# Performance work log

Hardware: AMD Instinct MI355X
Metric: run time of the kernel (lower is better)

## Reference

```python
import jax, jax.numpy as jnp
import numpy as np

BN_EPS = 1e-5


def setup_inputs() -> dict:
    key = jax.random.key(0)
    ks = jax.random.split(key, 8)
    b, c, h, w, d = 16, 256, 128, 128, 64
    x = jax.random.normal(ks[0], (b, c, h, w), dtype=jnp.float32)
    conv1_w = jax.random.normal(ks[1], (c, c), dtype=jnp.float32) * np.sqrt(2.0 / c)
    conv1_b = jax.random.normal(ks[2], (c,), dtype=jnp.float32) * 0.02
    mk_w = jax.random.normal(ks[3], (d, c), dtype=jnp.float32) * np.sqrt(2.0 / d)
    mv_w = jnp.transpose(mk_w)  # original ties mv.weight = mk.weight.permute(1,0,2)
    conv2_w = jax.random.normal(ks[4], (c, c), dtype=jnp.float32) * np.sqrt(2.0 / c)
    bn_gamma = jnp.ones((c,), dtype=jnp.float32)
    bn_beta = jnp.zeros((c,), dtype=jnp.float32)
    bn_mean = jax.random.normal(ks[5], (c,), dtype=jnp.float32) * 0.1
    bn_var = jax.random.uniform(ks[6], (c,), dtype=jnp.float32, minval=0.5, maxval=1.5)
    return {"x": x, "conv1_w": conv1_w, "conv1_b": conv1_b, "mk_w": mk_w,
            "mv_w": mv_w, "conv2_w": conv2_w, "bn_gamma": bn_gamma,
            "bn_beta": bn_beta, "bn_mean": bn_mean, "bn_var": bn_var}


def reference(x, conv1_w, conv1_b, mk_w, mv_w, conv2_w, bn_gamma, bn_beta, bn_mean, bn_var):
    b, c, h, w = x.shape
    n = h * w
    identity = x
    # conv1: 1x1 conv with bias -> [b, c, n]
    y = jnp.einsum('oc,bchw->bohw', conv1_w, x) + conv1_b[None, :, None, None]
    y = y.reshape(b, c, n)
    # external attention: mk projection [b, d, n]
    attn = jnp.einsum('dc,bcn->bdn', mk_w, y)
    attn = jax.nn.softmax(attn, axis=-1)              # softmax over spatial N
    attn = attn / (1e-9 + attn.sum(axis=1, keepdims=True))  # column-normalize over d
    # mv projection back to channels [b, c, n]
    z = jnp.einsum('cd,bdn->bcn', mv_w, attn)
    z = z.reshape(b, c, h, w)
    # conv2 (1x1, no bias) + BatchNorm (inference) + residual + relu
    z = jnp.einsum('oc,bchw->bohw', conv2_w, z)
    inv = bn_gamma / jnp.sqrt(bn_var + BN_EPS)
    z = z * inv[None, :, None, None] + (bn_beta - bn_mean * inv)[None, :, None, None]
    return jax.nn.relu(z + identity)
```

## Files before the change

### kernel.cpp

```cpp
#include <hip/hip_runtime.h>

#define HW 16384
#define C  256
#define D  64
#define NB 16

typedef unsigned short u16;
typedef __attribute__((ext_vector_type(4))) float  f32x4;
typedef __attribute__((ext_vector_type(4))) short  s16x4;
typedef __attribute__((ext_vector_type(8))) short  s16x8;

__device__ __forceinline__ float fast_exp(float v) {
    return exp2f(v * 1.44269504088896340736f);
}
__device__ __forceinline__ float bf2f(u16 u) {
    return __uint_as_float(((unsigned int)u) << 16);
}
__device__ __forceinline__ u16 f2bf(float f) {
    unsigned int u = __float_as_uint(f);
    unsigned int r = (u + 0x7fffu + ((u >> 16) & 1u)) >> 16;
    return (u16)r;
}

#define MFMA16(a, b, c) __builtin_amdgcn_mfma_f32_16x16x32_bf16((a), (b), (c), 0, 0, 0)

__global__ void precompute_kernel(const float* __restrict__ conv1_w,
                                  const float* __restrict__ conv1_b,
                                  const float* __restrict__ mk_w,
                                  const float* __restrict__ mv_w,
                                  const float* __restrict__ conv2_w,
                                  const float* __restrict__ gamma,
                                  const float* __restrict__ beta,
                                  const float* __restrict__ mean,
                                  const float* __restrict__ var,
                                  short* __restrict__ Ath,
                                  short* __restrict__ Atl,
                                  float* __restrict__ amk,
                                  short* __restrict__ Bmb,
                                  float* __restrict__ shift)
{
    int gid = blockIdx.x * blockDim.x + threadIdx.x;
    if (gid < C * D) {
        int d = gid >> 8, cp = gid & 255;
        float s = 0.f;
        for (int c = 0; c < C; ++c) s += mk_w[d * C + c] * conv1_w[c * C + cp];
        u16 h = f2bf(s);
        Ath[gid] = (short)h;
        Atl[gid] = (short)f2bf(s - bf2f(h));
    } else if (gid < 2 * C * D) {
        int g = gid - C * D;
        int o = g >> 6, d = g & 63;
        float inv = gamma[o] * rsqrtf(var[o] + 1e-5f);
        float s = 0.f;
        for (int c = 0; c < C; ++c) s += conv2_w[o * C + c] * mv_w[c * D + d];
        Bmb[g] = (short)f2bf(s * inv);
    } else if (gid < 2 * C * D + D) {
        int d = gid - 2 * C * D;
        float s = 0.f;
        for (int c = 0; c < C; ++c) s += mk_w[d * C + c] * conv1_b[c];
        amk[d] = s;
    } else if (gid < 2 * C * D + D + C) {
        int o = gid - (2 * C * D + D);
        float inv = gamma[o] * rsqrtf(var[o] + 1e-5f);
        shift[o] = beta[o] - mean[o] * inv;
    }
}

#define NT1 64
__global__ __launch_bounds__(256, 2) void logits_kernel(const float* __restrict__ x,
                                                        const short* __restrict__ Ath,
                                                        const short* __restrict__ Atl,
                                                        const float* __restrict__ amk,
                                                        u16* __restrict__ logits)
{
    __shared__ short xs[NT1][2 * C + 8];
    const int t = threadIdx.x;
    const int b = blockIdx.y;
    const int n0 = blockIdx.x * NT1;
    const int lane = t & 63, w = t >> 6;
    const int col = lane & 15, g = lane >> 4;

    s16x8 Ah[8], Al[8];
    {
        const short* ah = Ath + (size_t)(w * 16 + col) * C + 8 * g;
        const short* al = Atl + (size_t)(w * 16 + col) * C + 8 * g;
        #pragma unroll
        for (int ks = 0; ks < 8; ++ks) {
            Ah[ks] = *(const s16x8*)(ah + ks * 32);
            Al[ks] = *(const s16x8*)(al + ks * 32);
        }
    }

    const float* xb = x + (size_t)b * C * HW + n0;
    #pragma unroll
    for (int i = 0; i < 4; ++i) {
        int cell = i * 256 + t;
        int nq = cell & 15, cq = cell >> 4;
        int c0 = cq * 4, nn = nq * 4;
        const float* gp = xb + (size_t)c0 * HW + nn;
        f32x4 r0 = *(const f32x4*)(gp);
        f32x4 r1 = *(const f32x4*)(gp + HW);
        f32x4 r2 = *(const f32x4*)(gp + 2 * HW);
        f32x4 r3 = *(const f32x4*)(gp + 3 * HW);
        #pragma unroll
        for (int j = 0; j < 4; ++j) {
            float v0 = r0[j], v1 = r1[j], v2 = r2[j], v3 = r3[j];
            u16 h0 = f2bf(v0), h1 = f2bf(v1), h2 = f2bf(v2), h3 = f2bf(v3);
            s16x4 hi = { (short)h0, (short)h1, (short)h2, (short)h3 };
            s16x4 lo = { (short)f2bf(v0 - bf2f(h0)), (short)f2bf(v1 - bf2f(h1)),
                         (short)f2bf(v2 - bf2f(h2)), (short)f2bf(v3 - bf2f(h3)) };
            *(s16x4*)&xs[nn + j][c0]     = hi;
            *(s16x4*)&xs[nn + j][C + c0] = lo;
        }
    }
    __syncthreads();

    f32x4 zz = {0.f, 0.f, 0.f, 0.f};
    f32x4 acc[4] = { zz, zz, zz, zz };
    #pragma unroll
    for (int ks = 0; ks < 8; ++ks) {
        #pragma unroll
        for (int nt = 0; nt < 4; ++nt) {
            const short* xr = &xs[nt * 16 + col][ks * 32 + 8 * g];
            s16x8 bh = *(const s16x8*)(xr);
            s16x8 bl = *(const s16x8*)(xr + C);
            acc[nt] = MFMA16(Ah[ks], bh, acc[nt]);
            acc[nt] = MFMA16(Al[ks], bh, acc[nt]);
            acc[nt] = MFMA16(Ah[ks], bl, acc[nt]);
        }
    }

    f32x4 av = *(const f32x4*)(amk + w * 16 + 4 * g);
    u16* lb = logits + (size_t)b * D * HW + n0;
    #pragma unroll
    for (int nt = 0; nt < 4; ++nt) {
        #pragma unroll
        for (int r = 0; r < 4; ++r) {
            int d = w * 16 + 4 * g + r;
            lb[(size_t)d * HW + nt * 16 + col] = f2bf(acc[nt][r] + av[r]);
        }
    }
}

__global__ __launch_bounds__(256) void stats_kernel(const u16* __restrict__ logits,
                                                    float* __restrict__ stats)
{
    const int row = blockIdx.x;
    const u16* lr = logits + (size_t)row * HW;
    const int t = threadIdx.x;
    const int lane = t & 63, wid = t >> 6;

    float v[64];
    float m = -3.402823466e+38f;
    #pragma unroll
    for (int i = 0; i < 64; ++i) {
        v[i] = bf2f(lr[t + i * 256]);
        m = fmaxf(m, v[i]);
    }
    #pragma unroll
    for (int off = 1; off < 64; off <<= 1) m = fmaxf(m, __shfl_xor(m, off));

    __shared__ float redm[4];
    if (lane == 0) redm[wid] = m;
    __syncthreads();
    const float bm = fmaxf(fmaxf(redm[0], redm[1]), fmaxf(redm[2], redm[3]));

    float s = 0.f;
    #pragma unroll
    for (int i = 0; i < 64; ++i) s += fast_exp(v[i] - bm);
    #pragma unroll
    for (int off = 1; off < 64; off <<= 1) s += __shfl_xor(s, off);

    __shared__ float reds[4];
    if (lane == 0) reds[wid] = s;
    __syncthreads();
    if (t == 0) {
        float S = reds[0] + reds[1] + reds[2] + reds[3];
        stats[2 * row]     = bm;
        stats[2 * row + 1] = 1.0f / S;
    }
}

#define NT3 128
__global__ __launch_bounds__(512, 4) void out_kernel(const float* __restrict__ x,
                                                     const u16* __restrict__ logits,
                                                     const float* __restrict__ stats,
                                                     const short* __restrict__ Bmb,
                                                     const float* __restrict__ shift,
                                                     float* __restrict__ out)
{
    __shared__ short ps[NT3][72];
    __shared__ float csum[4][NT3];
    __shared__ float rr[NT3];

    const int t = threadIdx.x;
    const int b = blockIdx.y;
    const int n0 = blockIdx.x * NT3;

    {
        const int nl = t & 127, dq = t >> 7;
        const u16* lg = logits + (size_t)b * D * HW + (size_t)(dq * 16) * HW + n0 + nl;
        const float* st = stats + 2 * (b * D + dq * 16);
        float cs = 0.f;
        #pragma unroll
        for (int j4 = 0; j4 < 4; ++j4) {
            s16x4 pk;
            #pragma unroll
            for (int jj = 0; jj < 4; ++jj) {
                int j = j4 * 4 + jj;
                float M = st[2 * j], invS = st[2 * j + 1];
                float pv = fast_exp(bf2f(lg[(size_t)j * HW]) - M) * invS;
                cs += pv;
                pk[jj] = (short)f2bf(pv);
            }
            *(s16x4*)&ps[nl][dq * 16 + j4 * 4] = pk;
        }
        csum[dq][nl] = cs;
    }
    __syncthreads();
    if (t < NT3) {
        float s = csum[0][t] + csum[1][t] + csum[2][t] + csum[3][t] + 1e-9f;
        rr[t] = 1.0f / s;
    }
    __syncthreads();

    const int lane = t & 63, col = lane & 15, g = lane >> 4;
    const int W = t >> 6, Wo = W >> 1, Wn = W & 1;

    s16x8 A[4][2];
    #pragma unroll
    for (int ot = 0; ot < 4; ++ot) {
        const short* bp = Bmb + (size_t)(Wo * 64 + ot * 16 + col) * D + 8 * g;
        A[ot][0] = *(const s16x8*)(bp);
        A[ot][1] = *(const s16x8*)(bp + 32);
    }

    f32x4 zz = {0.f, 0.f, 0.f, 0.f};
    f32x4 acc[4][4];
    #pragma unroll
    for (int ot = 0; ot < 4; ++ot)
        #pragma unroll
        for (int nt = 0; nt < 4; ++nt) acc[ot][nt] = zz;

    #pragma unroll
    for (int nt = 0; nt < 4; ++nt) {
        const short* pr = &ps[Wn * 64 + nt * 16 + col][8 * g];
        s16x8 b0 = *(const s16x8*)(pr);
        s16x8 b1 = *(const s16x8*)(pr + 32);
        #pragma unroll
        for (int ot = 0; ot < 4; ++ot) {
            acc[ot][nt] = MFMA16(A[ot][0], b0, acc[ot][nt]);
            acc[ot][nt] = MFMA16(A[ot][1], b1, acc[ot][nt]);
        }
    }

    const float* xb = x + (size_t)b * C * HW + n0;
    float* ob = out + (size_t)b * C * HW + n0;
    #pragma unroll
    for (int ot = 0; ot < 4; ++ot) {
        f32x4 sh = *(const f32x4*)(shift + Wo * 64 + ot * 16 + 4 * g);
        #pragma unroll
        for (int nt = 0; nt < 4; ++nt) {
            int nc = Wn * 64 + nt * 16 + col;
            float rv = rr[nc];
            #pragma unroll
            for (int r = 0; r < 4; ++r) {
                int o = Wo * 64 + ot * 16 + 4 * g + r;
                float xv = xb[(size_t)o * HW + nc];
                float v = acc[ot][nt][r] * rv + sh[r] + xv;
                ob[(size_t)o * HW + nc] = fmaxf(v, 0.f);
            }
        }
    }
}

extern "C" void kernel_launch(void* const* d_in, const int* in_sizes, int n_in,
                              void* d_out, int out_size, void* d_ws, size_t ws_size,
                              hipStream_t stream)
{
    const float* x       = (const float*)d_in[0];
    const float* conv1_w = (const float*)d_in[1];
    const float* conv1_b = (const float*)d_in[2];
    const float* mk_w    = (const float*)d_in[3];
    const float* mv_w    = (const float*)d_in[4];
    const float* conv2_w = (const float*)d_in[5];
    const float* gamma   = (const float*)d_in[6];
    const float* beta    = (const float*)d_in[7];
    const float* mean    = (const float*)d_in[8];
    const float* var     = (const float*)d_in[9];
    float* out = (float*)d_out;

    float* amk   = (float*)d_ws;
    float* shift = amk + D;
    float* stats = shift + C;
    short* Ath   = (short*)(stats + 2 * NB * D);
    short* Atl   = Ath + C * D;
    short* Bmb   = Atl + C * D;
    u16* logits  = (u16*)(Bmb + C * D);

    const int pre_work = 2 * C * D + D + C;
    precompute_kernel<<<(pre_work + 255) / 256, 256, 0, stream>>>(
        conv1_w, conv1_b, mk_w, mv_w, conv2_w, gamma, beta, mean, var,
        Ath, Atl, amk, Bmb, shift);

    logits_kernel<<<dim3(HW / NT1, NB), 256, 0, stream>>>(x, Ath, Atl, amk, logits);

    stats_kernel<<<NB * D, 256, 0, stream>>>(logits, stats);

    out_kernel<<<dim3(HW / NT3, NB), 512, 0, stream>>>(x, logits, stats, Bmb, shift, out);
}
```

Before: 581.8 us.

## Swap MFMA operand roles for vectorized stores, drop x low-part split

The logits kernel now converts x to a single bf16 plane instead of hi/lo planes. It swaps the MFMA operands so that each lane's accumulator holds contiguous spatial positions, which lets it write logits as 4-wide vector stores, and it loads the weights after the shared-memory fill to lower register pressure. The stats kernel reads logits four at a time, and the out kernel uses 64-column tiles with 256 threads and the swapped operand order, so residual loads and output stores become float4. The costs removed are scalar strided global accesses and one third of the logits MFMAs; in exchange x is kept only to bf16 precision (no low part), which loosens logit accuracy.

Result: no change. 588.1 us (+1.1%).

```diff
diff --git a/kernel.cpp b/kernel.cpp
--- a/kernel.cpp
+++ b/kernel.cpp
@@ -67,29 +67,19 @@
 }
 
 #define NT1 64
-__global__ __launch_bounds__(256, 2) void logits_kernel(const float* __restrict__ x,
+#define XR  (C + 8)
+__global__ __launch_bounds__(256, 3) void logits_kernel(const float* __restrict__ x,
                                                         const short* __restrict__ Ath,
                                                         const short* __restrict__ Atl,
                                                         const float* __restrict__ amk,
                                                         u16* __restrict__ logits)
 {
-    __shared__ short xs[NT1][2 * C + 8];
+    __shared__ short xs[NT1 * XR];
     const int t = threadIdx.x;
     const int b = blockIdx.y;
     const int n0 = blockIdx.x * NT1;
     const int lane = t & 63, w = t >> 6;
     const int col = lane & 15, g = lane >> 4;
-
-    s16x8 Ah[8], Al[8];
-    {
-        const short* ah = Ath + (size_t)(w * 16 + col) * C + 8 * g;
-        const short* al = Atl + (size_t)(w * 16 + col) * C + 8 * g;
-        #pragma unroll
-        for (int ks = 0; ks < 8; ++ks) {
-            Ah[ks] = *(const s16x8*)(ah + ks * 32);
-            Al[ks] = *(const s16x8*)(al + ks * 32);
-        }
-    }
 
     const float* xb = x + (size_t)b * C * HW + n0;
     #pragma unroll
@@ -104,16 +94,23 @@
         f32x4 r3 = *(const f32x4*)(gp + 3 * HW);
         #pragma unroll
         for (int j = 0; j < 4; ++j) {
-            float v0 = r0[j], v1 = r1[j], v2 = r2[j], v3 = r3[j];
-            u16 h0 = f2bf(v0), h1 = f2bf(v1), h2 = f2bf(v2), h3 = f2bf(v3);
-            s16x4 hi = { (short)h0, (short)h1, (short)h2, (short)h3 };
-            s16x4 lo = { (short)f2bf(v0 - bf2f(h0)), (short)f2bf(v1 - bf2f(h1)),
-                         (short)f2bf(v2 - bf2f(h2)), (short)f2bf(v3 - bf2f(h3)) };
-            *(s16x4*)&xs[nn + j][c0]     = hi;
-            *(s16x4*)&xs[nn + j][C + c0] = lo;
-        }
-    }
-    __syncthreads();
+            s16x4 hi = { (short)f2bf(r0[j]), (short)f2bf(r1[j]),
+                         (short)f2bf(r2[j]), (short)f2bf(r3[j]) };
+            *(s16x4*)&xs[(nn + j) * XR + c0] = hi;
+        }
+    }
+    __syncthreads();
+
+    s16x8 Ah[8], Al[8];
+    {
+        const short* ah = Ath + (size_t)(w * 16 + col) * C + 8 * g;
+        const short* al = Atl + (size_t)(w * 16 + col) * C + 8 * g;
+        #pragma unroll
+        for (int ks = 0; ks < 8; ++ks) {
+            Ah[ks] = *(const s16x8*)(ah + ks * 32);
+            Al[ks] = *(const s16x8*)(al + ks * 32);
+        }
+    }
 
     f32x4 zz = {0.f, 0.f, 0.f, 0.f};
     f32x4 acc[4] = { zz, zz, zz, zz };
@@ -121,24 +118,20 @@
     for (int ks = 0; ks < 8; ++ks) {
         #pragma unroll
         for (int nt = 0; nt < 4; ++nt) {
-            const short* xr = &xs[nt * 16 + col][ks * 32 + 8 * g];
-            s16x8 bh = *(const s16x8*)(xr);
-            s16x8 bl = *(const s16x8*)(xr + C);
-            acc[nt] = MFMA16(Ah[ks], bh, acc[nt]);
-            acc[nt] = MFMA16(Al[ks], bh, acc[nt]);
-            acc[nt] = MFMA16(Ah[ks], bl, acc[nt]);
-        }
-    }
-
-    f32x4 av = *(const f32x4*)(amk + w * 16 + 4 * g);
-    u16* lb = logits + (size_t)b * D * HW + n0;
+            s16x8 xf = *(const s16x8*)&xs[(nt * 16 + col) * XR + ks * 32 + 8 * g];
+            acc[nt] = MFMA16(xf, Ah[ks], acc[nt]);
+            acc[nt] = MFMA16(xf, Al[ks], acc[nt]);
+        }
+    }
+
+    const float am = amk[w * 16 + col];
+    u16* lb = logits + (size_t)b * D * HW + (size_t)(w * 16 + col) * HW + n0;
     #pragma unroll
     for (int nt = 0; nt < 4; ++nt) {
-        #pragma unroll
-        for (int r = 0; r < 4; ++r) {
-            int d = w * 16 + 4 * g + r;
-            lb[(size_t)d * HW + nt * 16 + col] = f2bf(acc[nt][r] + av[r]);
-        }
+        s16x4 st4;
+        #pragma unroll
+        for (int r = 0; r < 4; ++r) st4[r] = (short)f2bf(acc[nt][r] + am);
+        *(s16x4*)(lb + nt * 16 + 4 * g) = st4;
     }
 }
 
@@ -146,16 +139,21 @@
                                                     float* __restrict__ stats)
 {
     const int row = blockIdx.x;
-    const u16* lr = logits + (size_t)row * HW;
+    const s16x4* lr = (const s16x4*)(logits + (size_t)row * HW);
     const int t = threadIdx.x;
     const int lane = t & 63, wid = t >> 6;
 
     float v[64];
     float m = -3.402823466e+38f;
     #pragma unroll
-    for (int i = 0; i < 64; ++i) {
-        v[i] = bf2f(lr[t + i * 256]);
-        m = fmaxf(m, v[i]);
+    for (int i = 0; i < 16; ++i) {
+        s16x4 q = lr[t + i * 256];
+        #pragma unroll
+        for (int k = 0; k < 4; ++k) {
+            float f = bf2f((u16)q[k]);
+            v[i * 4 + k] = f;
+            m = fmaxf(m, f);
+        }
     }
     #pragma unroll
     for (int off = 1; off < 64; off <<= 1) m = fmaxf(m, __shfl_xor(m, off));
@@ -181,15 +179,15 @@
     }
 }
 
-#define NT3 128
-__global__ __launch_bounds__(512, 4) void out_kernel(const float* __restrict__ x,
+#define NT3 64
+__global__ __launch_bounds__(256, 3) void out_kernel(const float* __restrict__ x,
                                                      const u16* __restrict__ logits,
                                                      const float* __restrict__ stats,
                                                      const short* __restrict__ Bmb,
                                                      const float* __restrict__ shift,
                                                      float* __restrict__ out)
 {
-    __shared__ short ps[NT3][72];
+    __shared__ short ps[NT3 * 72];
     __shared__ float csum[4][NT3];
     __shared__ float rr[NT3];
 
@@ -198,7 +196,7 @@
     const int n0 = blockIdx.x * NT3;
 
     {
-        const int nl = t & 127, dq = t >> 7;
+        const int nl = t & 63, dq = t >> 6;
         const u16* lg = logits + (size_t)b * D * HW + (size_t)(dq * 16) * HW + n0 + nl;
         const float* st = stats + 2 * (b * D + dq * 16);
         float cs = 0.f;
@@ -208,31 +206,28 @@
             #pragma unroll
             for (int jj = 0; jj < 4; ++jj) {
                 int j = j4 * 4 + jj;
-                float M = st[2 * j], invS = st[2 * j + 1];
-                float pv = fast_exp(bf2f(lg[(size_t)j * HW]) - M) * invS;
+                float pv = fast_exp(bf2f(lg[(size_t)j * HW]) - st[2 * j]) * st[2 * j + 1];
                 cs += pv;
                 pk[jj] = (short)f2bf(pv);
             }
-            *(s16x4*)&ps[nl][dq * 16 + j4 * 4] = pk;
+            *(s16x4*)&ps[nl * 72 + dq * 16 + j4 * 4] = pk;
         }
         csum[dq][nl] = cs;
     }
     __syncthreads();
-    if (t < NT3) {
-        float s = csum[0][t] + csum[1][t] + csum[2][t] + csum[3][t] + 1e-9f;
-        rr[t] = 1.0f / s;
-    }
+    if (t < NT3)
+        rr[t] = 1.0f / (csum[0][t] + csum[1][t] + csum[2][t] + csum[3][t] + 1e-9f);
     __syncthreads();
 
     const int lane = t & 63, col = lane & 15, g = lane >> 4;
-    const int W = t >> 6, Wo = W >> 1, Wn = W & 1;
-
-    s16x8 A[4][2];
+    const int w = t >> 6;
+
+    s16x8 Bf[4][2];
     #pragma unroll
     for (int ot = 0; ot < 4; ++ot) {
-        const short* bp = Bmb + (size_t)(Wo * 64 + ot * 16 + col) * D + 8 * g;
-        A[ot][0] = *(const s16x8*)(bp);
-        A[ot][1] = *(const s16x8*)(bp + 32);
+        const short* bp = Bmb + (size_t)(w * 64 + ot * 16 + col) * D + 8 * g;
+        Bf[ot][0] = *(const s16x8*)(bp);
+        Bf[ot][1] = *(const s16x8*)(bp + 32);
     }
 
     f32x4 zz = {0.f, 0.f, 0.f, 0.f};
@@ -244,32 +239,34 @@
 
     #pragma unroll
     for (int nt = 0; nt < 4; ++nt) {
-        const short* pr = &ps[Wn * 64 + nt * 16 + col][8 * g];
-        s16x8 b0 = *(const s16x8*)(pr);
-        s16x8 b1 = *(const s16x8*)(pr + 32);
+        const short* pr = &ps[(nt * 16 + col) * 72 + 8 * g];
+        s16x8 p0 = *(const s16x8*)(pr);
+        s16x8 p1 = *(const s16x8*)(pr + 32);
         #pragma unroll
         for (int ot = 0; ot < 4; ++ot) {
-            acc[ot][nt] = MFMA16(A[ot][0], b0, acc[ot][nt]);
-            acc[ot][nt] = MFMA16(A[ot][1], b1, acc[ot][nt]);
-        }
-    }
+            acc[ot][nt] = MFMA16(p0, Bf[ot][0], acc[ot][nt]);
+            acc[ot][nt] = MFMA16(p1, Bf[ot][1], acc[ot][nt]);
+        }
+    }
+
+    float sh[4];
+    #pragma unroll
+    for (int ot = 0; ot < 4; ++ot) sh[ot] = shift[w * 64 + ot * 16 + col];
 
     const float* xb = x + (size_t)b * C * HW + n0;
     float* ob = out + (size_t)b * C * HW + n0;
     #pragma unroll
-    for (int ot = 0; ot < 4; ++ot) {
-        f32x4 sh = *(const f32x4*)(shift + Wo * 64 + ot * 16 + 4 * g);
-        #pragma unroll
-        for (int nt = 0; nt < 4; ++nt) {
-            int nc = Wn * 64 + nt * 16 + col;
-            float rv = rr[nc];
+    for (int nt = 0; nt < 4; ++nt) {
+        f32x4 rv = *(const f32x4*)&rr[nt * 16 + 4 * g];
+        #pragma unroll
+        for (int ot = 0; ot < 4; ++ot) {
+            const size_t off = (size_t)(w * 64 + ot * 16 + col) * HW + nt * 16 + 4 * g;
+            f32x4 xv = *(const f32x4*)(xb + off);
+            f32x4 vv;
             #pragma unroll
-            for (int r = 0; r < 4; ++r) {
-                int o = Wo * 64 + ot * 16 + 4 * g + r;
-                float xv = xb[(size_t)o * HW + nc];
-                float v = acc[ot][nt][r] * rv + sh[r] + xv;
-                ob[(size_t)o * HW + nc] = fmaxf(v, 0.f);
-            }
+            for (int r = 0; r < 4; ++r)
+                vv[r] = fmaxf(acc[ot][nt][r] * rv[r] + sh[ot] + xv[r], 0.f);
+            *(f32x4*)(ob + off) = vv;
         }
     }
 }
@@ -307,5 +304,5 @@
 
     stats_kernel<<<NB * D, 256, 0, stream>>>(logits, stats);
 
-    out_kernel<<<dim3(HW / NT3, NB), 512, 0, stream>>>(x, logits, stats, Bmb, shift, out);
-}
+    out_kernel<<<dim3(HW / NT3, NB), 256, 0, stream>>>(x, logits, stats, Bmb, shift, out);
+}
```
